# Kernel optimization log

Hardware: AMD Instinct MI355X
Metric: run time of the kernel (lower is better)

Reference implementation:

```python
import jax, jax.numpy as jnp
import numpy as np

# Dims: T=64 steps, B=8 batch, H=128 hidden, NH=4 heads, D=2*H=256 cell dim
T, B, H, NH = 64, 8, 128, 4
D = 2 * H
EPS = 1e-5


def _bn(v, scale, bias):
    # flax BatchNorm (training mode): stats over all axes except feature (-1)
    axes = tuple(range(v.ndim - 1))
    mu = v.mean(axes, keepdims=True)
    var = v.var(axes, keepdims=True)
    return (v - mu) * jax.lax.rsqrt(var + EPS) * scale + bias


def setup_inputs() -> dict:
    key = jax.random.key(0)
    ks = iter(jax.random.split(key, 48))
    r = lambda shape, s=0.02: (jax.random.normal(next(ks), shape, jnp.float32) * s)
    z = lambda shape: jnp.zeros(shape, jnp.float32)
    o = lambda shape: jnp.ones(shape, jnp.float32)
    inp = {
        "x": jax.random.normal(next(ks), (T, B, H), jnp.float32),
        # per-head mLSTMCell params (stacked over NH heads), flax Linear: y = x @ W + b
        "Wq": r((NH, D, D)), "bq": z((NH, D)),
        "Wk": r((NH, D, D)), "bk": z((NH, D)),
        "Wv": r((NH, D, D)), "bv": z((NH, D)),
        "conv_k": r((4, 1, NH), 0.2), "conv_b": z((NH,)),  # 1->NH channel conv == per-head 1->1 conv
        "Wi": r((NH, D)), "bi": r((NH,), 0.01),
        "Wf": r((NH, D)),
        "bf": jax.random.uniform(next(ks), (NH,), jnp.float32, 3.0, 6.0),
        "Wo": r((NH, D, D)), "bo": z((NH, D)),
        "Wskip": r((NH, D, D)), "bskip": z((NH, D)),
        # block params
        "bn1_s": o((H,)), "bn1_b": z((H,)),
        "bn2_s": o((D,)), "bn2_b": z((D,)),
        "Wup1": r((H, D)), "bup1": z((D,)),
        "Wup2": r((H, D)), "bup2": z((D,)),
        "Wpoll": r((NH * D, D)), "bpoll": z((D,)),
        "Wdown": r((D, H)), "bdown": z((H,)),
    }
    return inp


def reference(x, Wq, bq, Wk, bk, Wv, bv, conv_k, conv_b, Wi, bi, Wf, bf,
              Wo, bo, Wskip, bskip, bn1_s, bn1_b, bn2_s, bn2_b,
              Wup1, bup1, Wup2, bup2, Wpoll, bpoll, Wdown, bdown):
    nh, d, _ = Wq.shape
    b = x.shape[1]
    inv_sqrt_d = 1.0 / jnp.sqrt(jnp.float32(d))

    def step(carry, xt):
        c, n, m = carry  # c: [nh,b,d,d], n: [nh,b,d], m: [nh,b]
        u = _bn(xt, bn1_s, bn1_b)                      # [b,H]
        trig = jax.nn.silu(u @ Wup2 + bup2)            # [b,d]
        xin = u @ Wup1 + bup1                          # [b,d] mlstm input
        outg = jax.nn.sigmoid(jnp.einsum('bd,hde->hbe', xin, Wo) + bo[:, None, :])
        it = jnp.einsum('bd,hd->hb', xin, Wi) + bi[:, None]
        ft = jnp.einsum('bd,hd->hb', xin, Wf) + bf[:, None]
        m_new = jnp.maximum(ft + m, it)
        ig = jnp.exp(it - m_new)
        fg = jnp.exp(ft + m - m_new)
        # causal-ish depthwise conv over feature axis (flax Conv SAME, k=4)
        qk = jax.lax.conv_general_dilated(xin[..., None], conv_k, (1,), 'SAME',
                                          dimension_numbers=('NWC', 'WIO', 'NWC')) + conv_b
        qk = jax.nn.silu(jnp.transpose(qk, (2, 0, 1)))  # [nh,b,d]
        k = (jnp.einsum('hbd,hde->hbe', qk, Wk) + bk[:, None, :]) * inv_sqrt_d
        q = jnp.einsum('hbd,hde->hbe', qk, Wq) + bq[:, None, :]
        v = jnp.einsum('bd,hde->hbe', xin, Wv) + bv[:, None, :]
        c_new = fg[:, :, None, None] * c + jnp.einsum('hb,hbi,hbj->hbij', ig, v, k)
        n_new = fg[..., None] * n + ig[..., None] * k
        scaler = 1.0 / jnp.maximum(jnp.abs(jnp.einsum('hbi,hbi->hb', n_new, q)), 1.0)
        h = outg * jnp.einsum('hbik,hbk->hbi', c_new, q) * scaler[..., None]
        h = h + jnp.einsum('hbd,hde->hbe', qk, Wskip) + bskip[:, None, :]
        ho = _bn(h, bn2_s, bn2_b)                      # [nh,b,d]
        ho = jnp.transpose(ho, (1, 0, 2)).reshape(b, nh * d)
        ho = ho @ Wpoll + bpoll                        # [b,d]
        y = (ho * trig) @ Wdown + bdown + xt           # residual
        return (c_new, n_new, m_new), y

    c0 = jnp.zeros((nh, b, d, d), x.dtype)
    n0 = jnp.zeros((nh, b, d), x.dtype)
    m0 = jnp.zeros((nh, b), x.dtype)
    _, ys = jax.lax.scan(step, (c0, n0, m0), x)
    return ys
```

## Files before the change

### kernel.cpp

```cpp
#include <hip/hip_runtime.h>
#include <hip/hip_bf16.h>

#define T_ 64
#define B_ 8
#define H_ 128
#define NH_ 4
#define D_ 256
#define TB_ 512
#define EPS_ 1e-5f

typedef short bf16x8 __attribute__((ext_vector_type(8)));
typedef float f32x4 __attribute__((ext_vector_type(4)));

__device__ __forceinline__ float silu_(float x){ return x / (1.0f + __expf(-x)); }
__device__ __forceinline__ float sigm_(float x){ return 1.0f / (1.0f + __expf(-x)); }
__device__ __forceinline__ unsigned short tobf_(float f){
  unsigned u = __float_as_uint(f);
  u += 0x7FFF + ((u >> 16) & 1);
  return (unsigned short)(u >> 16);
}
__device__ __forceinline__ int afrag_(int m, int k){
  return (((m >> 4)*8 + (k >> 5))*64 + ((k >> 3)&3)*16 + (m & 15))*8 + (k & 7);
}
__device__ __forceinline__ int afrag1024_(int m, int k){
  return (((m >> 4)*32 + (k >> 5))*64 + ((k >> 3)&3)*16 + (m & 15))*8 + (k & 7);
}

__global__ __launch_bounds__(256) void k_prep(
    const float* __restrict__ Wq, const float* __restrict__ Wk, const float* __restrict__ Ws,
    const float* __restrict__ Wv, const float* __restrict__ Wo,
    const float* __restrict__ Wup1, const float* __restrict__ Wup2,
    const float* __restrict__ Wp, const float* __restrict__ Wd,
    const float* __restrict__ x, const float* __restrict__ bn1s, const float* __restrict__ bn1b,
    unsigned short* __restrict__ Wqt, unsigned short* __restrict__ Wkt,
    unsigned short* __restrict__ Wst, unsigned short* __restrict__ Wvt,
    unsigned short* __restrict__ Wot,
    unsigned short* __restrict__ Wu1t, unsigned short* __restrict__ Wu2t,
    unsigned short* __restrict__ Wpt, unsigned short* __restrict__ Wdt,
    unsigned short* __restrict__ ub){
  int bid = blockIdx.x;
  int tid = threadIdx.x;
  if (bid < 640){
    int sub = bid & 31;
    int h   = (bid >> 5) & 3;
    int mat = bid >> 7;
    const float* Win; unsigned short* Wout;
    switch (mat){
      case 0: Win = Wq; Wout = Wqt; break;
      case 1: Win = Wk; Wout = Wkt; break;
      case 2: Win = Ws; Wout = Wst; break;
      case 3: Win = Wv; Wout = Wvt; break;
      default: Win = Wo; Wout = Wot; break;
    }
    Win  += h * (D_*D_);
    Wout += h * (D_*D_);
    int gid = sub*256 + tid;
    int combo = gid >> 6;
    int l = gid & 63;
    int lm = l & 15, lq = l >> 4;
    int nt = combo >> 3, kb = combo & 7;
    int n = nt*16 + lm;
    int k0 = kb*32 + lq*8;
    bf16x8 v;
    #pragma unroll
    for (int j = 0; j < 8; j++) v[j] = (short)tobf_(Win[(k0+j)*D_ + n]);
    *(bf16x8*)(Wout + (combo*64 + l)*8) = v;
  } else if (bid < 672){
    int idx = bid - 640;
    const float* Win = (idx < 16) ? Wup1 : Wup2;
    unsigned short* Wout = (idx < 16) ? Wu1t : Wu2t;
    int sub = idx & 15;
    int gid = sub*256 + tid;
    int combo = gid >> 6;
    int l = gid & 63;
    int lm = l & 15, lq = l >> 4;
    int nt = combo >> 2, kb = combo & 3;
    int n = nt*16 + lm;
    int k0 = kb*32 + lq*8;
    bf16x8 v;
    #pragma unroll
    for (int j = 0; j < 8; j++) v[j] = (short)tobf_(Win[(k0+j)*D_ + n]);
    *(bf16x8*)(Wout + (combo*64 + l)*8) = v;
  } else if (bid < 704){
    int i = bid - 672;
    int tt = tid >> 7, hf = tid & 127;
    int t = i*2 + tt;
    const float* xp = x + t*(B_*H_) + hf;
    float v0[8]; float mu = 0.f;
    #pragma unroll
    for (int b = 0; b < 8; b++){ v0[b] = xp[b*H_]; mu += v0[b]; }
    mu *= 0.125f;
    float var = 0.f;
    #pragma unroll
    for (int b = 0; b < 8; b++){ float dd = v0[b]-mu; var += dd*dd; }
    var *= 0.125f;
    float sc = (1.0f/sqrtf(var + EPS_)) * bn1s[hf];
    float bs = bn1b[hf];
    int kb = hf >> 5, j = hf & 7;
    int lanebase = ((hf >> 3)&3)*16 + tt*8;
    unsigned short* up = ub + ((i*4 + kb)*64)*8 + j;
    #pragma unroll
    for (int b = 0; b < 8; b++)
      up[(lanebase + b)*8] = tobf_((v0[b]-mu)*sc + bs);
  } else if (bid < 832){
    int gid = (bid - 704)*256 + tid;
    int combo = gid >> 6;
    int l = gid & 63;
    int lm = l & 15, lq = l >> 4;
    int nt = combo >> 5, kb = combo & 31;
    int n = nt*16 + lm;
    int k0 = kb*32 + lq*8;
    bf16x8 v;
    #pragma unroll
    for (int j = 0; j < 8; j++) v[j] = (short)tobf_(Wp[(k0+j)*D_ + n]);
    *(bf16x8*)(Wpt + (combo*64 + l)*8) = v;
  } else {
    int gid = (bid - 832)*256 + tid;
    int combo = gid >> 6;
    int l = gid & 63;
    int lm = l & 15, lq = l >> 4;
    int nt = combo >> 3, kb = combo & 7;
    int n = nt*16 + lm;
    int k0 = kb*32 + lq*8;
    bf16x8 v;
    #pragma unroll
    for (int j = 0; j < 8; j++) v[j] = (short)tobf_(Wd[(k0+j)*H_ + n]);
    *(bf16x8*)(Wdt + (combo*64 + l)*8) = v;
  }
}

__global__ __launch_bounds__(256) void k_upcg(
    const unsigned short* __restrict__ ub,
    const unsigned short* __restrict__ Wu1t, const unsigned short* __restrict__ Wu2t,
    const float* __restrict__ bup1, const float* __restrict__ bup2,
    const float* __restrict__ ck, const float* __restrict__ cb,
    const float* __restrict__ Wi, const float* __restrict__ bi,
    const float* __restrict__ Wf, const float* __restrict__ bfv,
    unsigned short* __restrict__ xinb, unsigned short* __restrict__ qkb,
    float* __restrict__ trig, float* __restrict__ itb, float* __restrict__ ftb){
  __shared__ float xs[16][257];
  int bid = blockIdx.x;
  int mat = bid >> 5, rt = bid & 31;
  int tid = threadIdx.x;
  int w = tid >> 6, l = tid & 63, lm = l & 15, lq = l >> 4;
  const unsigned short* Bt = (mat == 0) ? Wu1t : Wu2t;
  f32x4 acc[4];
  #pragma unroll
  for (int nt = 0; nt < 4; nt++) acc[nt] = (f32x4){0.f,0.f,0.f,0.f};
  const unsigned short* Ap = ub + l*8;
  const unsigned short* Bp = Bt + l*8;
  #pragma unroll
  for (int kb = 0; kb < 4; kb++){
    bf16x8 a = *(const bf16x8*)(Ap + ((rt*4 + kb) << 9));
    #pragma unroll
    for (int nt = 0; nt < 4; nt++){
      bf16x8 bfr = *(const bf16x8*)(Bp + (((w*4+nt)*4 + kb) << 9));
      acc[nt] = __builtin_amdgcn_mfma_f32_16x16x32_bf16(a, bfr, acc[nt], 0, 0, 0);
    }
  }
  const float* bias = (mat == 0) ? bup1 : bup2;
  #pragma unroll
  for (int nt = 0; nt < 4; nt++){
    #pragma unroll
    for (int r = 0; r < 4; r++){
      int m = lq*4 + r;
      int row = rt*16 + m;
      int e = w*64 + nt*16 + lm;
      float vv = acc[nt][r] + bias[e];
      if (mat == 1){
        trig[row*D_ + e] = silu_(vv);
      } else {
        xinb[afrag_(row, e)] = tobf_(vv);
        xs[m][e] = vv;
      }
    }
  }
  if (mat == 0){
    __syncthreads();
    int d = tid;
    #pragma unroll 4
    for (int m = 0; m < 16; m++){
      float x0  = xs[m][d];
      float xm1 = (d >= 1)   ? xs[m][d-1] : 0.f;
      float xp1 = (d <= 254) ? xs[m][d+1] : 0.f;
      float xp2 = (d <= 253) ? xs[m][d+2] : 0.f;
      int rowg = rt*16 + m;
      int fa = afrag_(rowg, d);
      #pragma unroll
      for (int h = 0; h < NH_; h++){
        float a2 = cb[h];
        a2 = fmaf(xm1, ck[0*NH_+h], a2);
        a2 = fmaf(x0,  ck[1*NH_+h], a2);
        a2 = fmaf(xp1, ck[2*NH_+h], a2);
        a2 = fmaf(xp2, ck[3*NH_+h], a2);
        qkb[h*(TB_*D_) + fa] = tobf_(silu_(a2));
      }
    }
    int dot = tid >> 2, l4 = tid & 3;
    int h = dot >> 4, m = dot & 15;
    float ai = 0.f, af = 0.f;
    const float* wi = Wi + h*D_;
    const float* wf = Wf + h*D_;
    #pragma unroll 8
    for (int jj = 0; jj < 64; jj++){
      int k = l4*64 + jj;
      float xv = xs[m][k];
      ai = fmaf(xv, wi[k], ai);
      af = fmaf(xv, wf[k], af);
    }
    ai += __shfl_down(ai, 1); af += __shfl_down(af, 1);
    ai += __shfl_down(ai, 2); af += __shfl_down(af, 2);
    if (l4 == 0){
      int rowg = rt*16 + m;
      int t = rowg >> 3, b = rowg & 7;
      itb[(h*B_ + b)*T_ + t] = ai + bi[h];
      ftb[(h*B_ + b)*T_ + t] = af + bfv[h];
    }
  }
}

__global__ __launch_bounds__(256) void k_gemm5(
    const unsigned short* __restrict__ qkb, const unsigned short* __restrict__ xinb,
    const unsigned short* __restrict__ Wqt, const unsigned short* __restrict__ Wkt,
    const unsigned short* __restrict__ Wst, const unsigned short* __restrict__ Wvt,
    const unsigned short* __restrict__ Wot,
    const float* __restrict__ bq, const float* __restrict__ bk, const float* __restrict__ bsk,
    const float* __restrict__ bv, const float* __restrict__ bo,
    unsigned short* __restrict__ qob, unsigned short* __restrict__ kob,
    unsigned short* __restrict__ vot,
    float* __restrict__ hb, float* __restrict__ og){
  int bid = blockIdx.x;
  int rt  = bid & 15;
  int h   = (bid >> 4) & 3;
  int mat = bid >> 6;
  int tid = threadIdx.x;
  int w = tid >> 6, l = tid & 63;
  int lm = l & 15, lq = l >> 4;
  int r0 = rt * 32;
  const unsigned short* A = (mat < 3) ? (qkb + h*(TB_*D_)) : xinb;
  const unsigned short* Bt;
  const float* bias;
  switch (mat){
    case 0: Bt = Wqt; bias = bq;  break;
    case 1: Bt = Wkt; bias = bk;  break;
    case 2: Bt = Wst; bias = bsk; break;
    case 3: Bt = Wvt; bias = bv;  break;
    default: Bt = Wot; bias = bo; break;
  }
  Bt += h*(D_*D_);
  f32x4 acc[2][4];
  #pragma unroll
  for (int mt = 0; mt < 2; mt++)
    #pragma unroll
    for (int nt = 0; nt < 4; nt++) acc[mt][nt] = (f32x4){0.f,0.f,0.f,0.f};
  const unsigned short* Ap = A + l*8;
  const unsigned short* Bp = Bt + l*8;
  #pragma unroll
  for (int kc = 0; kc < 8; kc++){
    bf16x8 a0 = *(const bf16x8*)(Ap + ((rt*16      + kc) << 9));
    bf16x8 a1 = *(const bf16x8*)(Ap + ((rt*16 + 8  + kc) << 9));
    bf16x8 b0 = *(const bf16x8*)(Bp + (((w*4+0)*8 + kc) << 9));
    bf16x8 b1 = *(const bf16x8*)(Bp + (((w*4+1)*8 + kc) << 9));
    bf16x8 b2 = *(const bf16x8*)(Bp + (((w*4+2)*8 + kc) << 9));
    bf16x8 b3 = *(const bf16x8*)(Bp + (((w*4+3)*8 + kc) << 9));
    acc[0][0] = __builtin_amdgcn_mfma_f32_16x16x32_bf16(a0, b0, acc[0][0], 0, 0, 0);
    acc[0][1] = __builtin_amdgcn_mfma_f32_16x16x32_bf16(a0, b1, acc[0][1], 0, 0, 0);
    acc[0][2] = __builtin_amdgcn_mfma_f32_16x16x32_bf16(a0, b2, acc[0][2], 0, 0, 0);
    acc[0][3] = __builtin_amdgcn_mfma_f32_16x16x32_bf16(a0, b3, acc[0][3], 0, 0, 0);
    acc[1][0] = __builtin_amdgcn_mfma_f32_16x16x32_bf16(a1, b0, acc[1][0], 0, 0, 0);
    acc[1][1] = __builtin_amdgcn_mfma_f32_16x16x32_bf16(a1, b1, acc[1][1], 0, 0, 0);
    acc[1][2] = __builtin_amdgcn_mfma_f32_16x16x32_bf16(a1, b2, acc[1][2], 0, 0, 0);
    acc[1][3] = __builtin_amdgcn_mfma_f32_16x16x32_bf16(a1, b3, acc[1][3], 0, 0, 0);
  }
  float bval[4];
  #pragma unroll
  for (int nt = 0; nt < 4; nt++) bval[nt] = bias[h*D_ + w*64 + nt*16 + lm];
  #pragma unroll
  for (int mt = 0; mt < 2; mt++){
    #pragma unroll
    for (int r = 0; r < 4; r++){
      int row = r0 + mt*16 + lq*4 + r;
      int t = row >> 3, b = row & 7;
      #pragma unroll
      for (int nt = 0; nt < 4; nt++){
        int e = w*64 + nt*16 + lm;
        float vv = acc[mt][nt][r] + bval[nt];
        if (mat <= 1){
          if (mat == 1) vv *= 0.0625f;
          unsigned short* ob = (mat == 0) ? qob : kob;
          int mt2 = t >> 4, kb2 = e >> 5;
          int lane2 = ((e >> 3)&3)*16 + (t & 15);
          ob[(h*B_ + b)*16384 + ((mt2*8 + kb2)*64 + lane2)*8 + (e & 7)] = tobf_(vv);
        } else if (mat == 3){
          int nt3 = e >> 4, kb3 = t >> 5;
          int lane3 = ((t >> 3)&3)*16 + lm;
          vot[(h*B_ + b)*16384 + ((nt3*2 + kb3)*64 + lane3)*8 + (t & 7)] = tobf_(vv);
        } else {
          int obase = (((t*NH_ + h)*B_ + b) << 8) + e;
          if (mat == 4) og[obase] = sigm_(vv);
          else          hb[obase] = vv;
        }
      }
    }
  }
}

__global__ __launch_bounds__(256) void k_attn2(
    const unsigned short* __restrict__ qob, const unsigned short* __restrict__ kob,
    const unsigned short* __restrict__ vot, const float* __restrict__ og,
    const float* __restrict__ itb, const float* __restrict__ ftb,
    float* __restrict__ hb){
  __shared__ unsigned short Pf[1024];
  __shared__ float partial[4][16];
  __shared__ float scal[16];
  int bid = blockIdx.x;
  int hbx = bid >> 2, tq = bid & 3;
  int h = hbx >> 3, b = hbx & 7;
  int tid = threadIdx.x;
  int w = tid >> 6, l = tid & 63, lm = l & 15, lq = l >> 4;
  float F  = ftb[hbx*T_ + l];
  float it = itb[hbx*T_ + l];
  #pragma unroll
  for (int off = 1; off < 64; off <<= 1){
    float v2 = __shfl_up(F, off);
    if (l >= off) F += v2;
  }
  float ct = it - F;
  float G = ct;
  #pragma unroll
  for (int off = 1; off < 64; off <<= 1){
    float v2 = __shfl_up(G, off);
    if (l >= off) G = fmaxf(G, v2);
  }
  float rb = -fmaxf(0.f, G);
  const unsigned short* Aq = qob + hbx*16384 + l*8;
  const unsigned short* Bk = kob + hbx*16384 + l*8;
  f32x4 accs = (f32x4){0.f,0.f,0.f,0.f};
  #pragma unroll
  for (int kc = 0; kc < 8; kc++){
    bf16x8 a  = *(const bf16x8*)(Aq + ((tq*8 + kc) << 9));
    bf16x8 bb = *(const bf16x8*)(Bk + ((w*8  + kc) << 9));
    accs = __builtin_amdgcn_mfma_f32_16x16x32_bf16(a, bb, accs, 0, 0, 0);
  }
  int s = w*16 + lm;
  float ct_s = __shfl(ct, s);
  float p[4], ps[4];
  #pragma unroll
  for (int r = 0; r < 4; r++){
    int t = tq*16 + lq*4 + r;
    float rb_t = __shfl(rb, t);
    float pv = (s <= t) ? __expf(ct_s + rb_t) * accs[r] : 0.f;
    p[r] = pv; ps[r] = pv;
  }
  #pragma unroll
  for (int off = 1; off < 16; off <<= 1){
    #pragma unroll
    for (int r = 0; r < 4; r++) ps[r] += __shfl_xor(ps[r], off);
  }
  if (lm == 0){
    #pragma unroll
    for (int r = 0; r < 4; r++) partial[w][lq*4 + r] = ps[r];
  }
  {
    int kbP = w >> 1;
    int laneP = ((w*2 + (lm >> 3)) & 3)*16;
    int jP = lm & 7;
    #pragma unroll
    for (int r = 0; r < 4; r++){
      int m = lq*4 + r;
      Pf[(kbP*64 + laneP + m)*8 + jP] = tobf_(p[r]);
    }
  }
  __syncthreads();
  if (tid < 16){
    float sum = partial[0][tid] + partial[1][tid] + partial[2][tid] + partial[3][tid];
    scal[tid] = 1.0f / fmaxf(fabsf(sum), 1.0f);
  }
  bf16x8 pa0 = *(const bf16x8*)(Pf + l*8);
  bf16x8 pa1 = *(const bf16x8*)(Pf + 512 + l*8);
  const unsigned short* Bv = vot + hbx*16384 + l*8;
  f32x4 acco[4];
  #pragma unroll
  for (int nt = 0; nt < 4; nt++) acco[nt] = (f32x4){0.f,0.f,0.f,0.f};
  #pragma unroll
  for (int nt = 0; nt < 4; nt++){
    int nt3 = w*4 + nt;
    bf16x8 b0 = *(const bf16x8*)(Bv + (((nt3*2 + 0)) << 9));
    bf16x8 b1 = *(const bf16x8*)(Bv + (((nt3*2 + 1)) << 9));
    acco[nt] = __builtin_amdgcn_mfma_f32_16x16x32_bf16(pa0, b0, acco[nt], 0, 0, 0);
    acco[nt] = __builtin_amdgcn_mfma_f32_16x16x32_bf16(pa1, b1, acco[nt], 0, 0, 0);
  }
  __syncthreads();
  #pragma unroll
  for (int nt = 0; nt < 4; nt++){
    #pragma unroll
    for (int r = 0; r < 4; r++){
      int tl = lq*4 + r;
      int t = tq*16 + tl;
      int e = (w*4 + nt)*16 + lm;
      int idx = (((t*NH_ + h)*B_ + b) << 8) + e;
      hb[idx] += og[idx] * acco[nt][r] * scal[tl];
    }
  }
}

__global__ __launch_bounds__(256) void k_bn2f(
    const float* __restrict__ hbuf, const float* __restrict__ bn2s, const float* __restrict__ bn2b,
    unsigned short* __restrict__ hob){
  int t = blockIdx.x;
  int d = threadIdx.x;
  const float* hp = hbuf + (t*NH_*B_)*D_ + d;
  float v[32]; float mu = 0.f;
  #pragma unroll
  for (int i = 0; i < 32; i++){ v[i] = hp[i*D_]; mu += v[i]; }
  mu *= (1.0f/32.0f);
  float var = 0.f;
  #pragma unroll
  for (int i = 0; i < 32; i++){ float dd = v[i]-mu; var += dd*dd; }
  var *= (1.0f/32.0f);
  float sc = (1.0f/sqrtf(var + EPS_)) * bn2s[d];
  float bs = bn2b[d];
  #pragma unroll
  for (int i = 0; i < 32; i++){
    int hh = i >> 3, b = i & 7;
    int m = t*B_ + b;
    int k = hh*D_ + d;
    hob[afrag1024_(m, k)] = tobf_((v[i]-mu)*sc + bs);
  }
}

__global__ __launch_bounds__(512) void k_tail2(
    const unsigned short* __restrict__ hob, const unsigned short* __restrict__ Wpt,
    const float* __restrict__ bp, const float* __restrict__ trig,
    const unsigned short* __restrict__ Wdt, const float* __restrict__ bd,
    const float* __restrict__ x, float* __restrict__ y){
  __shared__ unsigned short zf[32*256];
  int rt = blockIdx.x;
  int tid = threadIdx.x;
  int w = tid >> 6, l = tid & 63, lm = l & 15, lq = l >> 4;
  f32x4 acc[2][2];
  #pragma unroll
  for (int mt = 0; mt < 2; mt++)
    #pragma unroll
    for (int nt = 0; nt < 2; nt++) acc[mt][nt] = (f32x4){0.f,0.f,0.f,0.f};
  const unsigned short* Ap = hob + l*8;
  const unsigned short* Bp = Wpt + l*8;
  #pragma unroll 4
  for (int kc = 0; kc < 32; kc++){
    bf16x8 a0 = *(const bf16x8*)(Ap + (((rt*2+0)*32 + kc) << 9));
    bf16x8 a1 = *(const bf16x8*)(Ap + (((rt*2+1)*32 + kc) << 9));
    bf16x8 b0 = *(const bf16x8*)(Bp + (((w*2+0)*32 + kc) << 9));
    bf16x8 b1 = *(const bf16x8*)(Bp + (((w*2+1)*32 + kc) << 9));
    acc[0][0] = __builtin_amdgcn_mfma_f32_16x16x32_bf16(a0, b0, acc[0][0], 0, 0, 0);
    acc[0][1] = __builtin_amdgcn_mfma_f32_16x16x32_bf16(a0, b1, acc[0][1], 0, 0, 0);
    acc[1][0] = __builtin_amdgcn_mfma_f32_16x16x32_bf16(a1, b0, acc[1][0], 0, 0, 0);
    acc[1][1] = __builtin_amdgcn_mfma_f32_16x16x32_bf16(a1, b1, acc[1][1], 0, 0, 0);
  }
  #pragma unroll
  for (int mt = 0; mt < 2; mt++){
    #pragma unroll
    for (int nt = 0; nt < 2; nt++){
      int e = w*32 + nt*16 + lm;
      float bpe = bp[e];
      #pragma unroll
      for (int r = 0; r < 4; r++){
        int ml = mt*16 + lq*4 + r;
        int row = rt*32 + ml;
        float z = (acc[mt][nt][r] + bpe) * trig[row*D_ + e];
        zf[afrag_(ml, e)] = tobf_(z);
      }
    }
  }
  __syncthreads();
  f32x4 acc2[2];
  acc2[0] = (f32x4){0.f,0.f,0.f,0.f};
  acc2[1] = (f32x4){0.f,0.f,0.f,0.f};
  const unsigned short* Bdp = Wdt + l*8;
  #pragma unroll
  for (int kc = 0; kc < 8; kc++){
    bf16x8 a0 = *(const bf16x8*)(zf + ((0*8 + kc) << 9) + l*8);
    bf16x8 a1 = *(const bf16x8*)(zf + ((1*8 + kc) << 9) + l*8);
    bf16x8 bb = *(const bf16x8*)(Bdp + ((w*8 + kc) << 9));
    acc2[0] = __builtin_amdgcn_mfma_f32_16x16x32_bf16(a0, bb, acc2[0], 0, 0, 0);
    acc2[1] = __builtin_amdgcn_mfma_f32_16x16x32_bf16(a1, bb, acc2[1], 0, 0, 0);
  }
  int hh = w*16 + lm;
  float bde = bd[hh];
  #pragma unroll
  for (int mt = 0; mt < 2; mt++){
    #pragma unroll
    for (int r = 0; r < 4; r++){
      int row = rt*32 + mt*16 + lq*4 + r;
      y[row*H_ + hh] = acc2[mt][r] + bde + x[row*H_ + hh];
    }
  }
}

extern "C" void kernel_launch(void* const* d_in, const int* in_sizes, int n_in,
                              void* d_out, int out_size, void* d_ws, size_t ws_size,
                              hipStream_t stream){
  const float* x     = (const float*)d_in[0];
  const float* Wq    = (const float*)d_in[1];
  const float* bq    = (const float*)d_in[2];
  const float* Wk    = (const float*)d_in[3];
  const float* bk    = (const float*)d_in[4];
  const float* Wv    = (const float*)d_in[5];
  const float* bv    = (const float*)d_in[6];
  const float* ck    = (const float*)d_in[7];
  const float* cb    = (const float*)d_in[8];
  const float* Wi    = (const float*)d_in[9];
  const float* bi    = (const float*)d_in[10];
  const float* Wf    = (const float*)d_in[11];
  const float* bf    = (const float*)d_in[12];
  const float* Wo    = (const float*)d_in[13];
  const float* bo    = (const float*)d_in[14];
  const float* Wsk   = (const float*)d_in[15];
  const float* bsk   = (const float*)d_in[16];
  const float* bn1s  = (const float*)d_in[17];
  const float* bn1b  = (const float*)d_in[18];
  const float* bn2s  = (const float*)d_in[19];
  const float* bn2b  = (const float*)d_in[20];
  const float* Wup1  = (const float*)d_in[21];
  const float* bup1  = (const float*)d_in[22];
  const float* Wup2  = (const float*)d_in[23];
  const float* bup2  = (const float*)d_in[24];
  const float* Wp    = (const float*)d_in[25];
  const float* bp    = (const float*)d_in[26];
  const float* Wd    = (const float*)d_in[27];
  const float* bd    = (const float*)d_in[28];
  float* y = (float*)d_out;

  float* w = (float*)d_ws;
  float* trig = w;  w += T_*B_*D_;
  float* hbuf = w;  w += T_*NH_*B_*D_;
  float* og   = w;  w += T_*NH_*B_*D_;
  float* itb  = w;  w += NH_*B_*T_;
  float* ftb  = w;  w += NH_*B_*T_;
  unsigned short* xinb = (unsigned short*)w;  w += (T_*B_*D_)/2;
  unsigned short* qkb  = (unsigned short*)w;  w += (NH_*TB_*D_)/2;
  unsigned short* Wqt  = (unsigned short*)w;  w += (NH_*D_*D_)/2;
  unsigned short* Wkt  = (unsigned short*)w;  w += (NH_*D_*D_)/2;
  unsigned short* Wst  = (unsigned short*)w;  w += (NH_*D_*D_)/2;
  unsigned short* Wvt  = (unsigned short*)w;  w += (NH_*D_*D_)/2;
  unsigned short* Wot  = (unsigned short*)w;  w += (NH_*D_*D_)/2;
  unsigned short* Wu1t = (unsigned short*)w;  w += (H_*D_)/2;
  unsigned short* Wu2t = (unsigned short*)w;  w += (H_*D_)/2;
  unsigned short* ub   = (unsigned short*)w;  w += (TB_*H_)/2;
  unsigned short* qob  = (unsigned short*)w;  w += (NH_*B_*T_*D_)/2;
  unsigned short* kob  = (unsigned short*)w;  w += (NH_*B_*T_*D_)/2;
  unsigned short* vot  = (unsigned short*)w;  w += (NH_*B_*T_*D_)/2;
  unsigned short* hob  = (unsigned short*)w;  w += (TB_*NH_*D_)/2;
  unsigned short* Wpt  = (unsigned short*)w;  w += (NH_*D_*D_)/2;
  unsigned short* Wdt  = (unsigned short*)w;  w += (D_*H_)/2;

  k_prep <<<848, 256, 0, stream>>>(Wq, Wk, Wsk, Wv, Wo, Wup1, Wup2, Wp, Wd, x, bn1s, bn1b,
                                   Wqt, Wkt, Wst, Wvt, Wot, Wu1t, Wu2t, Wpt, Wdt, ub);
  k_upcg <<<64, 256, 0, stream>>>(ub, Wu1t, Wu2t, bup1, bup2, ck, cb, Wi, bi, Wf, bf,
                                  xinb, qkb, trig, itb, ftb);
  k_gemm5<<<320, 256, 0, stream>>>(qkb, xinb, Wqt, Wkt, Wst, Wvt, Wot,
                                   bq, bk, bsk, bv, bo, qob, kob, vot, hbuf, og);
  k_attn2<<<NH_*B_*4, 256, 0, stream>>>(qob, kob, vot, og, itb, ftb, hbuf);
  k_bn2f <<<T_, 256, 0, stream>>>(hbuf, bn2s, bn2b, hob);
  k_tail2<<<16, 512, 0, stream>>>(hob, Wpt, bp, trig, Wdt, bd, x, y);
}
```

Baseline: 156.8 us.

## Fuse up-projection into prep kernel and BN2 into tail GEMM kernel

Merges the BN1/up-projection/conv/gate kernel into the weight-prep kernel: its blocks compute BN1 into shared memory and convert Wup1/Wup2 to bf16 on the fly, so the separate launch and the ub/Wu1t/Wu2t round trips through global memory go away. It also fuses BN2 into the tail kernel, which now normalizes two timesteps per block into shared memory before the Wpoll and Wdown GEMMs, removing another launch and the hob buffer. Together this drops two kernel launches. The cost is that each up-projection block redundantly reads fp32 weights with strided access, and the tail now runs 32 blocks of 256 threads where it used to run 16 blocks of 512.

```diff
diff --git a/kernel.cpp b/kernel.cpp
--- a/kernel.cpp
+++ b/kernel.cpp
@@ -26,24 +26,134 @@
   return (((m >> 4)*32 + (k >> 5))*64 + ((k >> 3)&3)*16 + (m & 15))*8 + (k & 7);
 }
 
-__global__ __launch_bounds__(256) void k_prep(
+__global__ __launch_bounds__(256) void k_prepup(
     const float* __restrict__ Wq, const float* __restrict__ Wk, const float* __restrict__ Ws,
     const float* __restrict__ Wv, const float* __restrict__ Wo,
     const float* __restrict__ Wup1, const float* __restrict__ Wup2,
     const float* __restrict__ Wp, const float* __restrict__ Wd,
     const float* __restrict__ x, const float* __restrict__ bn1s, const float* __restrict__ bn1b,
+    const float* __restrict__ bup1, const float* __restrict__ bup2,
+    const float* __restrict__ ck, const float* __restrict__ cb,
+    const float* __restrict__ Wi, const float* __restrict__ bi,
+    const float* __restrict__ Wf, const float* __restrict__ bfv,
     unsigned short* __restrict__ Wqt, unsigned short* __restrict__ Wkt,
     unsigned short* __restrict__ Wst, unsigned short* __restrict__ Wvt,
     unsigned short* __restrict__ Wot,
-    unsigned short* __restrict__ Wu1t, unsigned short* __restrict__ Wu2t,
     unsigned short* __restrict__ Wpt, unsigned short* __restrict__ Wdt,
-    unsigned short* __restrict__ ub){
+    unsigned short* __restrict__ xinb, unsigned short* __restrict__ qkb,
+    float* __restrict__ trig, float* __restrict__ itb, float* __restrict__ ftb){
+  __shared__ float xs[16][257];
+  __shared__ unsigned short ubl[2048];
   int bid = blockIdx.x;
   int tid = threadIdx.x;
-  if (bid < 640){
-    int sub = bid & 31;
-    int h   = (bid >> 5) & 3;
-    int mat = bid >> 7;
+  if (bid < 64){
+    int u = bid;
+    int mat = u >> 5, rt = u & 31;
+    {
+      int tt = tid >> 7, hf = tid & 127;
+      int t = rt*2 + tt;
+      const float* xp = x + t*(B_*H_) + hf;
+      float v0[8]; float mu = 0.f;
+      #pragma unroll
+      for (int b = 0; b < 8; b++){ v0[b] = xp[b*H_]; mu += v0[b]; }
+      mu *= 0.125f;
+      float var = 0.f;
+      #pragma unroll
+      for (int b = 0; b < 8; b++){ float dd = v0[b]-mu; var += dd*dd; }
+      var *= 0.125f;
+      float sc = (1.0f/sqrtf(var + EPS_)) * bn1s[hf];
+      float bs = bn1b[hf];
+      int kb = hf >> 5, j = hf & 7;
+      int lanebase = ((hf >> 3)&3)*16 + tt*8;
+      unsigned short* up = ubl + kb*512 + j;
+      #pragma unroll
+      for (int b = 0; b < 8; b++)
+        up[(lanebase + b)*8] = tobf_((v0[b]-mu)*sc + bs);
+    }
+    __syncthreads();
+    int w = tid >> 6, l = tid & 63, lm = l & 15, lq = l >> 4;
+    const float* Wf32 = (mat == 0) ? Wup1 : Wup2;
+    f32x4 acc[4];
+    #pragma unroll
+    for (int nt = 0; nt < 4; nt++) acc[nt] = (f32x4){0.f,0.f,0.f,0.f};
+    #pragma unroll
+    for (int kb = 0; kb < 4; kb++){
+      bf16x8 a = *(const bf16x8*)(ubl + kb*512 + l*8);
+      int k0 = kb*32 + lq*8;
+      #pragma unroll
+      for (int nt = 0; nt < 4; nt++){
+        int n = (w*4 + nt)*16 + lm;
+        const float* src = Wf32 + k0*D_ + n;
+        bf16x8 bfr;
+        #pragma unroll
+        for (int j = 0; j < 8; j++) bfr[j] = (short)tobf_(src[j*D_]);
+        acc[nt] = __builtin_amdgcn_mfma_f32_16x16x32_bf16(a, bfr, acc[nt], 0, 0, 0);
+      }
+    }
+    const float* bias = (mat == 0) ? bup1 : bup2;
+    #pragma unroll
+    for (int nt = 0; nt < 4; nt++){
+      #pragma unroll
+      for (int r = 0; r < 4; r++){
+        int m = lq*4 + r;
+        int row = rt*16 + m;
+        int e = w*64 + nt*16 + lm;
+        float vv = acc[nt][r] + bias[e];
+        if (mat == 1){
+          trig[row*D_ + e] = silu_(vv);
+        } else {
+          xinb[afrag_(row, e)] = tobf_(vv);
+          xs[m][e] = vv;
+        }
+      }
+    }
+    if (mat == 0){
+      __syncthreads();
+      int d = tid;
+      #pragma unroll 4
+      for (int m = 0; m < 16; m++){
+        float x0  = xs[m][d];
+        float xm1 = (d >= 1)   ? xs[m][d-1] : 0.f;
+        float xp1 = (d <= 254) ? xs[m][d+1] : 0.f;
+        float xp2 = (d <= 253) ? xs[m][d+2] : 0.f;
+        int rowg = rt*16 + m;
+        int fa = afrag_(rowg, d);
+        #pragma unroll
+        for (int h = 0; h < NH_; h++){
+          float a2 = cb[h];
+          a2 = fmaf(xm1, ck[0*NH_+h], a2);
+          a2 = fmaf(x0,  ck[1*NH_+h], a2);
+          a2 = fmaf(xp1, ck[2*NH_+h], a2);
+          a2 = fmaf(xp2, ck[3*NH_+h], a2);
+          qkb[h*(TB_*D_) + fa] = tobf_(silu_(a2));
+        }
+      }
+      int dot = tid >> 2, l4 = tid & 3;
+      int h = dot >> 4, m = dot & 15;
+      float ai = 0.f, af = 0.f;
+      const float* wi = Wi + h*D_;
+      const float* wf = Wf + h*D_;
+      #pragma unroll 8
+      for (int jj = 0; jj < 64; jj++){
+        int k = l4*64 + jj;
+        float xv = xs[m][k];
+        ai = fmaf(xv, wi[k], ai);
+        af = fmaf(xv, wf[k], af);
+      }
+      ai += __shfl_down(ai, 1); af += __shfl_down(af, 1);
+      ai += __shfl_down(ai, 2); af += __shfl_down(af, 2);
+      if (l4 == 0){
+        int rowg = rt*16 + m;
+        int t = rowg >> 3, b = rowg & 7;
+        itb[(h*B_ + b)*T_ + t] = ai + bi[h];
+        ftb[(h*B_ + b)*T_ + t] = af + bfv[h];
+      }
+    }
+  } else if (bid < 704){
+    int u = bid - 64;
+    int sub = u & 31;
+    int h   = (u >> 5) & 3;
+    int mat = u >> 7;
     const float* Win; unsigned short* Wout;
     switch (mat){
       case 0: Win = Wq; Wout = Wqt; break;
@@ -65,43 +175,6 @@
     #pragma unroll
     for (int j = 0; j < 8; j++) v[j] = (short)tobf_(Win[(k0+j)*D_ + n]);
     *(bf16x8*)(Wout + (combo*64 + l)*8) = v;
-  } else if (bid < 672){
-    int idx = bid - 640;
-    const float* Win = (idx < 16) ? Wup1 : Wup2;
-    unsigned short* Wout = (idx < 16) ? Wu1t : Wu2t;
-    int sub = idx & 15;
-    int gid = sub*256 + tid;
-    int combo = gid >> 6;
-    int l = gid & 63;
-    int lm = l & 15, lq = l >> 4;
-    int nt = combo >> 2, kb = combo & 3;
-    int n = nt*16 + lm;
-    int k0 = kb*32 + lq*8;
-    bf16x8 v;
-    #pragma unroll
-    for (int j = 0; j < 8; j++) v[j] = (short)tobf_(Win[(k0+j)*D_ + n]);
-    *(bf16x8*)(Wout + (combo*64 + l)*8) = v;
-  } else if (bid < 704){
-    int i = bid - 672;
-    int tt = tid >> 7, hf = tid & 127;
-    int t = i*2 + tt;
-    const float* xp = x + t*(B_*H_) + hf;
-    float v0[8]; float mu = 0.f;
-    #pragma unroll
-    for (int b = 0; b < 8; b++){ v0[b] = xp[b*H_]; mu += v0[b]; }
-    mu *= 0.125f;
-    float var = 0.f;
-    #pragma unroll
-    for (int b = 0; b < 8; b++){ float dd = v0[b]-mu; var += dd*dd; }
-    var *= 0.125f;
-    float sc = (1.0f/sqrtf(var + EPS_)) * bn1s[hf];
-    float bs = bn1b[hf];
-    int kb = hf >> 5, j = hf & 7;
-    int lanebase = ((hf >> 3)&3)*16 + tt*8;
-    unsigned short* up = ub + ((i*4 + kb)*64)*8 + j;
-    #pragma unroll
-    for (int b = 0; b < 8; b++)
-      up[(lanebase + b)*8] = tobf_((v0[b]-mu)*sc + bs);
   } else if (bid < 832){
     int gid = (bid - 704)*256 + tid;
     int combo = gid >> 6;
@@ -126,96 +199,6 @@
     #pragma unroll
     for (int j = 0; j < 8; j++) v[j] = (short)tobf_(Wd[(k0+j)*H_ + n]);
     *(bf16x8*)(Wdt + (combo*64 + l)*8) = v;
-  }
-}
-
-__global__ __launch_bounds__(256) void k_upcg(
-    const unsigned short* __restrict__ ub,
-    const unsigned short* __restrict__ Wu1t, const unsigned short* __restrict__ Wu2t,
-    const float* __restrict__ bup1, const float* __restrict__ bup2,
-    const float* __restrict__ ck, const float* __restrict__ cb,
-    const float* __restrict__ Wi, const float* __restrict__ bi,
-    const float* __restrict__ Wf, const float* __restrict__ bfv,
-    unsigned short* __restrict__ xinb, unsigned short* __restrict__ qkb,
-    float* __restrict__ trig, float* __restrict__ itb, float* __restrict__ ftb){
-  __shared__ float xs[16][257];
-  int bid = blockIdx.x;
-  int mat = bid >> 5, rt = bid & 31;
-  int tid = threadIdx.x;
-  int w = tid >> 6, l = tid & 63, lm = l & 15, lq = l >> 4;
-  const unsigned short* Bt = (mat == 0) ? Wu1t : Wu2t;
-  f32x4 acc[4];
-  #pragma unroll
-  for (int nt = 0; nt < 4; nt++) acc[nt] = (f32x4){0.f,0.f,0.f,0.f};
-  const unsigned short* Ap = ub + l*8;
-  const unsigned short* Bp = Bt + l*8;
-  #pragma unroll
-  for (int kb = 0; kb < 4; kb++){
-    bf16x8 a = *(const bf16x8*)(Ap + ((rt*4 + kb) << 9));
-    #pragma unroll
-    for (int nt = 0; nt < 4; nt++){
-      bf16x8 bfr = *(const bf16x8*)(Bp + (((w*4+nt)*4 + kb) << 9));
-      acc[nt] = __builtin_amdgcn_mfma_f32_16x16x32_bf16(a, bfr, acc[nt], 0, 0, 0);
-    }
-  }
-  const float* bias = (mat == 0) ? bup1 : bup2;
-  #pragma unroll
-  for (int nt = 0; nt < 4; nt++){
-    #pragma unroll
-    for (int r = 0; r < 4; r++){
-      int m = lq*4 + r;
-      int row = rt*16 + m;
-      int e = w*64 + nt*16 + lm;
-      float vv = acc[nt][r] + bias[e];
-      if (mat == 1){
-        trig[row*D_ + e] = silu_(vv);
-      } else {
-        xinb[afrag_(row, e)] = tobf_(vv);
-        xs[m][e] = vv;
-      }
-    }
-  }
-  if (mat == 0){
-    __syncthreads();
-    int d = tid;
-    #pragma unroll 4
-    for (int m = 0; m < 16; m++){
-      float x0  = xs[m][d];
-      float xm1 = (d >= 1)   ? xs[m][d-1] : 0.f;
-      float xp1 = (d <= 254) ? xs[m][d+1] : 0.f;
-      float xp2 = (d <= 253) ? xs[m][d+2] : 0.f;
-      int rowg = rt*16 + m;
-      int fa = afrag_(rowg, d);
-      #pragma unroll
-      for (int h = 0; h < NH_; h++){
-        float a2 = cb[h];
-        a2 = fmaf(xm1, ck[0*NH_+h], a2);
-        a2 = fmaf(x0,  ck[1*NH_+h], a2);
-        a2 = fmaf(xp1, ck[2*NH_+h], a2);
-        a2 = fmaf(xp2, ck[3*NH_+h], a2);
-        qkb[h*(TB_*D_) + fa] = tobf_(silu_(a2));
-      }
-    }
-    int dot = tid >> 2, l4 = tid & 3;
-    int h = dot >> 4, m = dot & 15;
-    float ai = 0.f, af = 0.f;
-    const float* wi = Wi + h*D_;
-    const float* wf = Wf + h*D_;
-    #pragma unroll 8
-    for (int jj = 0; jj < 64; jj++){
-      int k = l4*64 + jj;
-      float xv = xs[m][k];
-      ai = fmaf(xv, wi[k], ai);
-      af = fmaf(xv, wf[k], af);
-    }
-    ai += __shfl_down(ai, 1); af += __shfl_down(af, 1);
-    ai += __shfl_down(ai, 2); af += __shfl_down(af, 2);
-    if (l4 == 0){
-      int rowg = rt*16 + m;
-      int t = rowg >> 3, b = rowg & 7;
-      itb[(h*B_ + b)*T_ + t] = ai + bi[h];
-      ftb[(h*B_ + b)*T_ + t] = af + bfv[h];
-    }
   }
 }
 
@@ -404,71 +387,66 @@
   }
 }
 
-__global__ __launch_bounds__(256) void k_bn2f(
+__global__ __launch_bounds__(256) void k_tail3(
     const float* __restrict__ hbuf, const float* __restrict__ bn2s, const float* __restrict__ bn2b,
-    unsigned short* __restrict__ hob){
-  int t = blockIdx.x;
-  int d = threadIdx.x;
-  const float* hp = hbuf + (t*NH_*B_)*D_ + d;
-  float v[32]; float mu = 0.f;
-  #pragma unroll
-  for (int i = 0; i < 32; i++){ v[i] = hp[i*D_]; mu += v[i]; }
-  mu *= (1.0f/32.0f);
-  float var = 0.f;
-  #pragma unroll
-  for (int i = 0; i < 32; i++){ float dd = v[i]-mu; var += dd*dd; }
-  var *= (1.0f/32.0f);
-  float sc = (1.0f/sqrtf(var + EPS_)) * bn2s[d];
-  float bs = bn2b[d];
-  #pragma unroll
-  for (int i = 0; i < 32; i++){
-    int hh = i >> 3, b = i & 7;
-    int m = t*B_ + b;
-    int k = hh*D_ + d;
-    hob[afrag1024_(m, k)] = tobf_((v[i]-mu)*sc + bs);
-  }
-}
-
-__global__ __launch_bounds__(512) void k_tail2(
-    const unsigned short* __restrict__ hob, const unsigned short* __restrict__ Wpt,
-    const float* __restrict__ bp, const float* __restrict__ trig,
-    const unsigned short* __restrict__ Wdt, const float* __restrict__ bd,
-    const float* __restrict__ x, float* __restrict__ y){
-  __shared__ unsigned short zf[32*256];
-  int rt = blockIdx.x;
+    const unsigned short* __restrict__ Wpt, const float* __restrict__ bp,
+    const float* __restrict__ trig, const unsigned short* __restrict__ Wdt,
+    const float* __restrict__ bd, const float* __restrict__ x, float* __restrict__ y){
+  __shared__ unsigned short hfr[16384];
+  __shared__ unsigned short zf[4096];
+  int u = blockIdx.x;
   int tid = threadIdx.x;
   int w = tid >> 6, l = tid & 63, lm = l & 15, lq = l >> 4;
-  f32x4 acc[2][2];
-  #pragma unroll
-  for (int mt = 0; mt < 2; mt++)
-    #pragma unroll
-    for (int nt = 0; nt < 2; nt++) acc[mt][nt] = (f32x4){0.f,0.f,0.f,0.f};
-  const unsigned short* Ap = hob + l*8;
-  const unsigned short* Bp = Wpt + l*8;
+  #pragma unroll
+  for (int s = 0; s < 2; s++){
+    int pair = tid + (s << 8);
+    int tt = pair >> 8;
+    int d  = pair & 255;
+    int t  = u*2 + tt;
+    const float* hp = hbuf + (t*NH_*B_)*D_ + d;
+    float v[32]; float mu = 0.f;
+    #pragma unroll
+    for (int i = 0; i < 32; i++){ v[i] = hp[i*D_]; mu += v[i]; }
+    mu *= (1.0f/32.0f);
+    float var = 0.f;
+    #pragma unroll
+    for (int i = 0; i < 32; i++){ float dd = v[i]-mu; var += dd*dd; }
+    var *= (1.0f/32.0f);
+    float sc = (1.0f/sqrtf(var + EPS_)) * bn2s[d];
+    float bs = bn2b[d];
+    #pragma unroll
+    for (int i = 0; i < 32; i++){
+      int hh = i >> 3, b = i & 7;
+      int m = tt*8 + b;
+      int k = hh*D_ + d;
+      hfr[afrag1024_(m, k)] = tobf_((v[i]-mu)*sc + bs);
+    }
+  }
+  __syncthreads();
+  f32x4 acc[4];
+  #pragma unroll
+  for (int nt = 0; nt < 4; nt++) acc[nt] = (f32x4){0.f,0.f,0.f,0.f};
+  const unsigned short* Apl = hfr + l*8;
+  const unsigned short* Bp  = Wpt + l*8;
   #pragma unroll 4
   for (int kc = 0; kc < 32; kc++){
-    bf16x8 a0 = *(const bf16x8*)(Ap + (((rt*2+0)*32 + kc) << 9));
-    bf16x8 a1 = *(const bf16x8*)(Ap + (((rt*2+1)*32 + kc) << 9));
-    bf16x8 b0 = *(const bf16x8*)(Bp + (((w*2+0)*32 + kc) << 9));
-    bf16x8 b1 = *(const bf16x8*)(Bp + (((w*2+1)*32 + kc) << 9));
-    acc[0][0] = __builtin_amdgcn_mfma_f32_16x16x32_bf16(a0, b0, acc[0][0], 0, 0, 0);
-    acc[0][1] = __builtin_amdgcn_mfma_f32_16x16x32_bf16(a0, b1, acc[0][1], 0, 0, 0);
-    acc[1][0] = __builtin_amdgcn_mfma_f32_16x16x32_bf16(a1, b0, acc[1][0], 0, 0, 0);
-    acc[1][1] = __builtin_amdgcn_mfma_f32_16x16x32_bf16(a1, b1, acc[1][1], 0, 0, 0);
-  }
-  #pragma unroll
-  for (int mt = 0; mt < 2; mt++){
-    #pragma unroll
-    for (int nt = 0; nt < 2; nt++){
-      int e = w*32 + nt*16 + lm;
-      float bpe = bp[e];
-      #pragma unroll
-      for (int r = 0; r < 4; r++){
-        int ml = mt*16 + lq*4 + r;
-        int row = rt*32 + ml;
-        float z = (acc[mt][nt][r] + bpe) * trig[row*D_ + e];
-        zf[afrag_(ml, e)] = tobf_(z);
-      }
+    bf16x8 a = *(const bf16x8*)(Apl + (kc << 9));
+    #pragma unroll
+    for (int nt = 0; nt < 4; nt++){
+      bf16x8 bfr = *(const bf16x8*)(Bp + ((((w*4+nt)*32) + kc) << 9));
+      acc[nt] = __builtin_amdgcn_mfma_f32_16x16x32_bf16(a, bfr, acc[nt], 0, 0, 0);
+    }
+  }
+  #pragma unroll
+  for (int nt = 0; nt < 4; nt++){
+    int e = w*64 + nt*16 + lm;
+    float bpe = bp[e];
+    #pragma unroll
+    for (int r = 0; r < 4; r++){
+      int ml = lq*4 + r;
+      int row = u*16 + ml;
+      float z = (acc[nt][r] + bpe) * trig[row*D_ + e];
+      zf[afrag_(ml, e)] = tobf_(z);
     }
   }
   __syncthreads();
@@ -478,20 +456,21 @@
   const unsigned short* Bdp = Wdt + l*8;
   #pragma unroll
   for (int kc = 0; kc < 8; kc++){
-    bf16x8 a0 = *(const bf16x8*)(zf + ((0*8 + kc) << 9) + l*8);
-    bf16x8 a1 = *(const bf16x8*)(zf + ((1*8 + kc) << 9) + l*8);
-    bf16x8 bb = *(const bf16x8*)(Bdp + ((w*8 + kc) << 9));
-    acc2[0] = __builtin_amdgcn_mfma_f32_16x16x32_bf16(a0, bb, acc2[0], 0, 0, 0);
-    acc2[1] = __builtin_amdgcn_mfma_f32_16x16x32_bf16(a1, bb, acc2[1], 0, 0, 0);
-  }
-  int hh = w*16 + lm;
-  float bde = bd[hh];
-  #pragma unroll
-  for (int mt = 0; mt < 2; mt++){
+    bf16x8 a = *(const bf16x8*)(zf + (kc << 9) + l*8);
+    #pragma unroll
+    for (int q = 0; q < 2; q++){
+      bf16x8 bb = *(const bf16x8*)(Bdp + (((w*2+q)*8 + kc) << 9));
+      acc2[q] = __builtin_amdgcn_mfma_f32_16x16x32_bf16(a, bb, acc2[q], 0, 0, 0);
+    }
+  }
+  #pragma unroll
+  for (int q = 0; q < 2; q++){
+    int hh = (w*2+q)*16 + lm;
+    float bde = bd[hh];
     #pragma unroll
     for (int r = 0; r < 4; r++){
-      int row = rt*32 + mt*16 + lq*4 + r;
-      y[row*H_ + hh] = acc2[mt][r] + bde + x[row*H_ + hh];
+      int row = u*16 + lq*4 + r;
+      y[row*H_ + hh] = acc2[q][r] + bde + x[row*H_ + hh];
     }
   }
 }
@@ -543,23 +522,18 @@
   unsigned short* Wst  = (unsigned short*)w;  w += (NH_*D_*D_)/2;
   unsigned short* Wvt  = (unsigned short*)w;  w += (NH_*D_*D_)/2;
   unsigned short* Wot  = (unsigned short*)w;  w += (NH_*D_*D_)/2;
-  unsigned short* Wu1t = (unsigned short*)w;  w += (H_*D_)/2;
-  unsigned short* Wu2t = (unsigned short*)w;  w += (H_*D_)/2;
-  unsigned short* ub   = (unsigned short*)w;  w += (TB_*H_)/2;
   unsigned short* qob  = (unsigned short*)w;  w += (NH_*B_*T_*D_)/2;
   unsigned short* kob  = (unsigned short*)w;  w += (NH_*B_*T_*D_)/2;
   unsigned short* vot  = (unsigned short*)w;  w += (NH_*B_*T_*D_)/2;
-  unsigned short* hob  = (unsigned short*)w;  w += (TB_*NH_*D_)/2;
   unsigned short* Wpt  = (unsigned short*)w;  w += (NH_*D_*D_)/2;
   unsigned short* Wdt  = (unsigned short*)w;  w += (D_*H_)/2;
 
-  k_prep <<<848, 256, 0, stream>>>(Wq, Wk, Wsk, Wv, Wo, Wup1, Wup2, Wp, Wd, x, bn1s, bn1b,
-                                   Wqt, Wkt, Wst, Wvt, Wot, Wu1t, Wu2t, Wpt, Wdt, ub);
-  k_upcg <<<64, 256, 0, stream>>>(ub, Wu1t, Wu2t, bup1, bup2, ck, cb, Wi, bi, Wf, bf,
-                                  xinb, qkb, trig, itb, ftb);
+  k_prepup<<<848, 256, 0, stream>>>(Wq, Wk, Wsk, Wv, Wo, Wup1, Wup2, Wp, Wd,
+                                    x, bn1s, bn1b, bup1, bup2, ck, cb, Wi, bi, Wf, bf,
+                                    Wqt, Wkt, Wst, Wvt, Wot, Wpt, Wdt,
+                                    xinb, qkb, trig, itb, ftb);
   k_gemm5<<<320, 256, 0, stream>>>(qkb, xinb, Wqt, Wkt, Wst, Wvt, Wot,
                                    bq, bk, bsk, bv, bo, qob, kob, vot, hbuf, og);
   k_attn2<<<NH_*B_*4, 256, 0, stream>>>(qob, kob, vot, og, itb, ftb, hbuf);
-  k_bn2f <<<T_, 256, 0, stream>>>(hbuf, bn2s, bn2b, hob);
-  k_tail2<<<16, 512, 0, stream>>>(hob, Wpt, bp, trig, Wdt, bd, x, y);
-}
+  k_tail3<<<32, 256, 0, stream>>>(hbuf, bn2s, bn2b, Wpt, bp, trig, Wdt, bd, x, y);
+}
```

Measured after the change: 155.3 us. No clear change (-1.0%).
